# Optimization experiments

Measured on AMD Instinct MI355X. Metric: run time of the kernel, lower is better.

The kernel has to match this reference:

```python
import jax, jax.numpy as jnp
import numpy as np

B, T, D, H = 4, 1024, 1024, 16
HD = D // H
MAX_LEN = 1024


def _layernorm(x, g, b, eps=1e-5):
    mu = jnp.mean(x, axis=-1, keepdims=True)
    var = jnp.var(x, axis=-1, keepdims=True)
    return (x - mu) * jax.lax.rsqrt(var + eps) * g + b


def setup_inputs() -> dict:
    key = jax.random.key(0)
    ks = jax.random.split(key, 12)
    s = 1.0 / np.sqrt(D)
    return {
        "src": jax.random.normal(ks[0], (B, T, D), jnp.float32),
        "Wqkv": jax.random.uniform(ks[1], (D, 3 * D), jnp.float32, -s, s),
        "bqkv": jnp.zeros((3 * D,), jnp.float32),
        "Wo": jax.random.uniform(ks[2], (D, D), jnp.float32, -s, s),
        "bo": jnp.zeros((D,), jnp.float32),
        "rel_bias": 0.02 * jax.random.normal(ks[3], (H, 2 * MAX_LEN - 1), jnp.float32),
        "temperature": jnp.float32(1.0),
        "W1": jax.random.uniform(ks[4], (D, 4 * D), jnp.float32, -s, s),
        "b1": jnp.zeros((4 * D,), jnp.float32),
        "W2": jax.random.uniform(ks[5], (4 * D, D), jnp.float32, -1.0 / np.sqrt(4 * D), 1.0 / np.sqrt(4 * D)),
        "b2": jnp.zeros((D,), jnp.float32),
        "ff_scale": jnp.ones((1,), jnp.float32),
        "gamma1": jnp.ones((D,), jnp.float32),
        "beta1": jnp.zeros((D,), jnp.float32),
        "gamma2": jnp.ones((D,), jnp.float32),
        "beta2": jnp.zeros((D,), jnp.float32),
    }


def reference(src, Wqkv, bqkv, Wo, bo, rel_bias, temperature, W1, b1, W2, b2,
              ff_scale, gamma1, beta1, gamma2, beta2):
    b, t, c = src.shape
    # QKV projection -> [3, B, H, T, HD]
    qkv = (src @ Wqkv + bqkv).reshape(b, t, 3, H, HD).transpose(2, 0, 3, 1, 4)
    q, k, v = qkv[0], qkv[1], qkv[2]
    temp = jnp.maximum(temperature, 0.01)  # clamp(min=0.01)
    logits = jnp.einsum("bhqd,bhkd->bhqk", q, k) / temp
    # relative position bias gather: [H, T, T]
    pos = jnp.arange(t)
    rel = pos[None, :] - pos[:, None] + (t - 1)
    logits = logits + rel_bias[:, rel][None]
    attn_weights = jax.nn.softmax(logits, axis=-1)
    attn_out = jnp.einsum("bhqk,bhkd->bhqd", attn_weights, v)
    attn_out = attn_out.transpose(0, 2, 1, 3).reshape(b, t, c) @ Wo + bo
    x = _layernorm(src + attn_out, gamma1, beta1)
    ff = jax.nn.gelu(x @ W1 + b1, approximate=False) @ W2 + b2
    out = _layernorm(x + ff_scale * ff, gamma2, beta2)
    return (out, attn_weights)
```

## Files before the change

kernel.cpp:

```cpp
#include <hip/hip_runtime.h>
#include <math.h>

#define BB 4
#define TT 1024
#define DM 1024
#define NH 16
#define HD 64
#define DFF 4096
#define N3 3072

typedef unsigned short u16;
typedef __attribute__((ext_vector_type(4))) float f32x4;
typedef __attribute__((ext_vector_type(8))) short s16x8;

__device__ __forceinline__ u16 f2bf(float f) {
    union { float f; unsigned u; } v; v.f = f;
    unsigned u = v.u;
    u += 0x7fffu + ((u >> 16) & 1u);
    return (u16)(u >> 16);
}
__device__ __forceinline__ float bf2f(u16 h) {
    union { unsigned u; float f; } v; v.u = ((unsigned)h) << 16;
    return v.f;
}

__device__ __forceinline__ void async_copy16(const void* g, void* l) {
    __builtin_amdgcn_global_load_lds(
        (const __attribute__((address_space(1))) unsigned int*)g,
        (__attribute__((address_space(3))) unsigned int*)l, 16, 0, 0);
}

__global__ __launch_bounds__(256) void prep_kernel(const float* __restrict__ src,
                                                   u16* __restrict__ srcbf,
                                                   const float* __restrict__ Wqkv,
                                                   u16* __restrict__ WqkvT,
                                                   const float* __restrict__ Wo,
                                                   u16* __restrict__ WoT,
                                                   const float* __restrict__ W1,
                                                   u16* __restrict__ W1T,
                                                   const float* __restrict__ W2,
                                                   u16* __restrict__ W2T) {
    __shared__ float tile[32][33];
    int bid = blockIdx.x;
    int tid = threadIdx.x;
    if (bid < 4096) {
        int i = (bid * 256 + tid) * 4;
        float4 v = *(const float4*)(src + i);
        u16 pk[4] = {f2bf(v.x), f2bf(v.y), f2bf(v.z), f2bf(v.w)};
        *(uint2*)(srcbf + i) = *(uint2*)pk;
        return;
    }
    bid -= 4096;
    const float* in;
    u16* out;
    int R, C, bx, by;
    if (bid < 3072)        { in = Wqkv; out = WqkvT; R = DM;  C = N3;  bx = bid % 96;  by = bid / 96; }
    else if (bid < 4096)   { bid -= 3072; in = Wo; out = WoT; R = DM;  C = DM;  bx = bid % 32;  by = bid / 32; }
    else if (bid < 8192)   { bid -= 4096; in = W1; out = W1T; R = DM;  C = DFF; bx = bid % 128; by = bid / 128; }
    else                   { bid -= 8192; in = W2; out = W2T; R = DFF; C = DM;  bx = bid % 32;  by = bid / 32; }
    int c0 = bx * 32, r0 = by * 32;
    int tx = tid & 31, ty = tid >> 5;
    for (int i = 0; i < 4; i++)
        tile[ty + i * 8][tx] = in[(size_t)(r0 + ty + i * 8) * C + c0 + tx];
    __syncthreads();
    for (int i = 0; i < 4; i++)
        out[(size_t)(c0 + ty + i * 8) * R + r0 + tx] = f2bf(tile[tx][ty + i * 8]);
}

__global__ __launch_bounds__(256) void transpose_bf_kernel(const u16* __restrict__ inH,
                                                           u16* __restrict__ out, int R, int C) {
    __shared__ float tile[32][33];
    size_t boff = (size_t)blockIdx.z * R * C;
    int c0 = blockIdx.x * 32, r0 = blockIdx.y * 32;
    int tx = threadIdx.x & 31, ty = threadIdx.x >> 5;
    for (int i = 0; i < 4; i++) {
        int r = r0 + ty + i * 8, c = c0 + tx;
        tile[ty + i * 8][tx] = bf2f(inH[boff + (size_t)r * C + c]);
    }
    __syncthreads();
    for (int i = 0; i < 4; i++) {
        int rr = r0 + tx, cc = c0 + ty + i * 8;
        out[boff + (size_t)cc * R + rr] = f2bf(tile[tx][ty + i * 8]);
    }
}

template<int EPI, int NT>
__global__ __launch_bounds__(512, 2) void gemm256_kernel(const u16* __restrict__ A,
                                                         const u16* __restrict__ BT,
                                                         const float* __restrict__ bias,
                                                         void* __restrict__ out0v,
                                                         u16* __restrict__ out1,
                                                         u16* __restrict__ out2,
                                                         int M, int N, int Kstride) {
    __shared__ u16 As[4][8192];
    __shared__ u16 Bs[4][8192];
    const int tid = threadIdx.x;
    const int lane = tid & 63;
    const int wave = tid >> 6;
    const int quad = lane >> 4;
    const int l15 = lane & 15;
    const int wm = wave >> 2;
    const int wn = wave & 3;
    const int m0 = blockIdx.y * 256;
    const int n0 = blockIdx.x * 256;
    const int koff = blockIdx.z * (NT * 32);

    const int srow = wave * 32 + (lane >> 2);
    const int schunk = ((lane & 3) ^ ((lane >> 2) & 3)) * 8;
    const u16* aG0 = A + (size_t)(m0 + srow) * Kstride + koff + schunk;
    const u16* aG1 = aG0 + (size_t)16 * Kstride;
    const u16* bG0 = BT + (size_t)(n0 + srow) * Kstride + koff + schunk;
    const u16* bG1 = bG0 + (size_t)16 * Kstride;
    const int ldst0 = wave * 1024;
    const int ldst1 = wave * 1024 + 512;

#define STAGE_A(t) { int kk_ = (t) * 32; \
    async_copy16(aG0 + kk_, &As[(t) & 3][ldst0]); \
    async_copy16(aG1 + kk_, &As[(t) & 3][ldst1]); }
#define STAGE_B(t) { int kk_ = (t) * 32; \
    async_copy16(bG0 + kk_, &Bs[(t) & 3][ldst0]); \
    async_copy16(bG1 + kk_, &Bs[(t) & 3][ldst1]); }

    const int swq = (quad ^ (l15 & 3)) * 8;
    const int abase = (wm * 128 + l15) * 32 + swq;
    const int bbase = (wn * 64 + l15) * 32 + swq;

    f32x4 acc[8][4] = {};

    STAGE_A(0); STAGE_B(0);
    STAGE_A(1); STAGE_B(1);
    STAGE_A(2); STAGE_B(2);

#pragma unroll 1
    for (int t = 0; t < NT; ++t) {
        if (t < NT - 2)       asm volatile("s_waitcnt vmcnt(8)" ::: "memory");
        else if (t == NT - 2) asm volatile("s_waitcnt vmcnt(4)" ::: "memory");
        else                  asm volatile("s_waitcnt vmcnt(0)" ::: "memory");
        asm volatile("" ::: "memory");
        __builtin_amdgcn_s_barrier();
        asm volatile("" ::: "memory");

        const u16* as = As[t & 3];
        const u16* bs = Bs[t & 3];

        s16x8 bfr[4];
#pragma unroll
        for (int j = 0; j < 4; j++)
            bfr[j] = *(const s16x8*)&bs[bbase + j * 512];
        s16x8 afr[4];
#pragma unroll
        for (int i = 0; i < 4; i++)
            afr[i] = *(const s16x8*)&as[abase + i * 512];
        if (t + 3 < NT) STAGE_A(t + 3);
        __builtin_amdgcn_s_setprio(1);
#pragma unroll
        for (int i = 0; i < 4; i++)
#pragma unroll
            for (int j = 0; j < 4; j++)
                acc[i][j] = __builtin_amdgcn_mfma_f32_16x16x32_bf16(afr[i], bfr[j], acc[i][j], 0, 0, 0);
        __builtin_amdgcn_s_setprio(0);
#pragma unroll
        for (int i = 0; i < 4; i++)
            afr[i] = *(const s16x8*)&as[abase + 2048 + i * 512];
        if (t + 3 < NT) STAGE_B(t + 3);
        __builtin_amdgcn_s_setprio(1);
#pragma unroll
        for (int i = 0; i < 4; i++)
#pragma unroll
            for (int j = 0; j < 4; j++)
                acc[i + 4][j] = __builtin_amdgcn_mfma_f32_16x16x32_bf16(afr[i], bfr[j], acc[i + 4][j], 0, 0, 0);
        __builtin_amdgcn_s_setprio(0);
    }
#undef STAGE_A
#undef STAGE_B

    const size_t MN = (size_t)M * N;
#pragma unroll
    for (int i = 0; i < 8; i++) {
#pragma unroll
        for (int j = 0; j < 4; j++) {
            f32x4 c = acc[i][j];
            int gn = n0 + wn * 64 + j * 16 + l15;
            float bv = (EPI == 3) ? 0.f : bias[gn];
#pragma unroll
            for (int r = 0; r < 4; r++) {
                int gm = m0 + wm * 128 + i * 16 + quad * 4 + r;
                float v = c[r] + bv;
                if (EPI == 2) {
                    v = 0.5f * v * (1.f + erff(v * 0.70710678118f));
                    ((u16*)out0v)[(size_t)gm * N + gn] = f2bf(v);
                } else if (EPI == 3) {
                    ((float*)out0v)[(size_t)blockIdx.z * MN + (size_t)gm * N + gn] = v;
                } else {
                    int which = gn >> 10, h = (gn >> 6) & 15, d = gn & 63;
                    int bb = gm >> 10, tq = gm & 1023;
                    u16* dst = (which == 0) ? (u16*)out0v : ((which == 1) ? out1 : out2);
                    dst[((size_t)(bb * NH + h) * TT + tq) * HD + d] = f2bf(v);
                }
            }
        }
    }
}

__global__ __launch_bounds__(256) void attn_kernel(const u16* __restrict__ Qb,
                                                   const u16* __restrict__ Kb,
                                                   const u16* __restrict__ VTb,
                                                   const float* __restrict__ rel_bias,
                                                   const float* __restrict__ temp_p,
                                                   float* __restrict__ probs_out,
                                                   u16* __restrict__ attn_out) {
    __shared__ float RBs[1088];
    __shared__ unsigned Pl[4][16 * 20];

    const int tid = threadIdx.x;
    const int lane = tid & 63, wid = tid >> 6, quad = lane >> 4, l15 = lane & 15;
    const int q0b = blockIdx.x * 64;
    const int h = blockIdx.y, b = blockIdx.z;
    const int bh = b * NH + h;
    const size_t headoff = (size_t)bh * TT * HD;

    const float itemp = 1.f / fmaxf(temp_p[0], 0.01f);

    for (int i = tid; i < 1087; i += 256)
        RBs[i] = rel_bias[h * 2047 + (960 - q0b) + i];
    __syncthreads();

    const int qloc = wid * 16 + l15;
    const int qg = q0b + qloc;
    const u16* qp = Qb + headoff + (size_t)qg * HD;
    const s16x8 qa0 = *(const s16x8*)(qp + quad * 8);
    const s16x8 qa1 = *(const s16x8*)(qp + 32 + quad * 8);

    const u16* Kh = Kb + headoff;
    const int rbo = 63 - qloc;

    float m = -3.0e38f, l = 0.f;
#pragma unroll 2
    for (int kt = 0; kt < 64; kt++) {
        const u16* kp = Kh + (size_t)(kt * 16 + l15) * HD;
        s16x8 ka0 = *(const s16x8*)(kp + quad * 8);
        s16x8 ka1 = *(const s16x8*)(kp + 32 + quad * 8);
        f32x4 sv = {};
        sv = __builtin_amdgcn_mfma_f32_16x16x32_bf16(ka0, qa0, sv, 0, 0, 0);
        sv = __builtin_amdgcn_mfma_f32_16x16x32_bf16(ka1, qa1, sv, 0, 0, 0);
        int kb = kt * 16 + quad * 4 + rbo;
        float v0 = sv[0] * itemp + RBs[kb + 0];
        float v1 = sv[1] * itemp + RBs[kb + 1];
        float v2 = sv[2] * itemp + RBs[kb + 2];
        float v3 = sv[3] * itemp + RBs[kb + 3];
        float tm = fmaxf(fmaxf(v0, v1), fmaxf(v2, v3));
        float mn = fmaxf(m, tm);
        float c = __expf(m - mn);
        l = l * c + __expf(v0 - mn) + __expf(v1 - mn) + __expf(v2 - mn) + __expf(v3 - mn);
        m = mn;
    }
    float M = fmaxf(m, __shfl_xor(m, 16));
    M = fmaxf(M, __shfl_xor(M, 32));
    float la = l * __expf(m - M);
    la += __shfl_xor(la, 16);
    la += __shfl_xor(la, 32);
    const float inv = 1.f / la;

    f32x4 o[4] = {};
    unsigned* Pw = Pl[wid];
    const u16* Vh = VTb + headoff;
    float* prow = probs_out + ((size_t)bh * TT + qg) * TT;

#pragma unroll 1
    for (int c2 = 0; c2 < 32; c2++) {
        int k0 = c2 * 32;
#pragma unroll
        for (int t = 0; t < 2; t++) {
            int kt = 2 * c2 + t;
            const u16* kp = Kh + (size_t)(kt * 16 + l15) * HD;
            s16x8 ka0 = *(const s16x8*)(kp + quad * 8);
            s16x8 ka1 = *(const s16x8*)(kp + 32 + quad * 8);
            f32x4 sv = {};
            sv = __builtin_amdgcn_mfma_f32_16x16x32_bf16(ka0, qa0, sv, 0, 0, 0);
            sv = __builtin_amdgcn_mfma_f32_16x16x32_bf16(ka1, qa1, sv, 0, 0, 0);
            int kb = kt * 16 + quad * 4 + rbo;
            float p0 = __expf(sv[0] * itemp + RBs[kb + 0] - M) * inv;
            float p1 = __expf(sv[1] * itemp + RBs[kb + 1] - M) * inv;
            float p2 = __expf(sv[2] * itemp + RBs[kb + 2] - M) * inv;
            float p3 = __expf(sv[3] * itemp + RBs[kb + 3] - M) * inv;
            unsigned w0 = (unsigned)f2bf(p0) | ((unsigned)f2bf(p1) << 16);
            unsigned w1 = (unsigned)f2bf(p2) | ((unsigned)f2bf(p3) << 16);
            Pw[l15 * 20 + t * 8 + quad * 2 + 0] = w0;
            Pw[l15 * 20 + t * 8 + quad * 2 + 1] = w1;
        }
        s16x8 pb = *(const s16x8*)&Pw[l15 * 20 + quad * 4];
        f32x4 f0, f1;
#pragma unroll
        for (int j = 0; j < 4; j++) {
            f0[j] = bf2f((u16)pb[j]);
            f1[j] = bf2f((u16)pb[4 + j]);
        }
        *(f32x4*)(prow + k0 + quad * 8) = f0;
        *(f32x4*)(prow + k0 + quad * 8 + 4) = f1;
#pragma unroll
        for (int nt = 0; nt < 4; nt++) {
            s16x8 va = *(const s16x8*)(Vh + (size_t)(nt * 16 + l15) * TT + k0 + quad * 8);
            o[nt] = __builtin_amdgcn_mfma_f32_16x16x32_bf16(va, pb, o[nt], 0, 0, 0);
        }
    }

    u16* aout = attn_out + ((size_t)(b * TT + qg)) * DM + h * HD;
#pragma unroll
    for (int nt = 0; nt < 4; nt++) {
        u16 pk[4] = {f2bf(o[nt][0]), f2bf(o[nt][1]), f2bf(o[nt][2]), f2bf(o[nt][3])};
        *(uint2*)(aout + nt * 16 + quad * 4) = *(uint2*)pk;
    }
}

template<int MODE, int KS>
__global__ __launch_bounds__(256) void ln_kernel(const float* __restrict__ af32,
                                                 const u16* __restrict__ abf,
                                                 const float* __restrict__ part,
                                                 const float* __restrict__ biasN,
                                                 const float* __restrict__ scale_p,
                                                 const float* __restrict__ gamma,
                                                 const float* __restrict__ beta,
                                                 float* __restrict__ outf,
                                                 u16* __restrict__ outbf) {
    __shared__ float red[2][4];
    const size_t MN = (size_t)BB * TT * DM;
    int row = blockIdx.x;
    int tid = threadIdx.x;
    float sc = (MODE == 1) ? scale_p[0] : 1.f;
    int c0 = tid * 4;
    size_t base = (size_t)row * DM + c0;
    float4 a = *(const float4*)(biasN + c0);
    float acc[4] = {a.x, a.y, a.z, a.w};
#pragma unroll
    for (int kz = 0; kz < KS; kz++) {
        float4 p = *(const float4*)(part + kz * MN + base);
        acc[0] += p.x; acc[1] += p.y; acc[2] += p.z; acc[3] += p.w;
    }
    float x[4];
#pragma unroll
    for (int c = 0; c < 4; c++) {
        float b0 = (MODE == 0) ? af32[base + c] : bf2f(abf[base + c]);
        x[c] = b0 + sc * acc[c];
    }
    float s = x[0] + x[1] + x[2] + x[3];
    float sq = x[0] * x[0] + x[1] * x[1] + x[2] * x[2] + x[3] * x[3];
    for (int off = 32; off >= 1; off >>= 1) {
        s += __shfl_xor(s, off);
        sq += __shfl_xor(sq, off);
    }
    int wave = tid >> 6;
    if ((tid & 63) == 0) {
        red[0][wave] = s;
        red[1][wave] = sq;
    }
    __syncthreads();
    s = red[0][0] + red[0][1] + red[0][2] + red[0][3];
    sq = red[1][0] + red[1][1] + red[1][2] + red[1][3];
    float mu = s * (1.f / DM);
    float var = sq * (1.f / DM) - mu * mu;
    float rs = rsqrtf(var + 1e-5f);
#pragma unroll
    for (int c = 0; c < 4; c++) {
        float y = (x[c] - mu) * rs * gamma[c0 + c] + beta[c0 + c];
        if (MODE == 0) outbf[base + c] = f2bf(y);
        else outf[base + c] = y;
    }
}

#define OFF_SRCBF 0UL
#define OFF_WQKVT 8388608UL
#define OFF_WOT 14680064UL
#define OFF_W1T 16777216UL
#define OFF_W2T 25165824UL
#define OFF_Q 33554432UL
#define OFF_K 41943040UL
#define OFF_V 50331648UL
#define OFF_VT 58720256UL
#define OFF_ATTNO 67108864UL
#define OFF_XBF 83886080UL
#define OFF_H1 92274688UL
#define OFF_PART 134217728UL

extern "C" void kernel_launch(void* const* d_in, const int* in_sizes, int n_in,
                              void* d_out, int out_size, void* d_ws, size_t ws_size,
                              hipStream_t stream) {
    const float* src = (const float*)d_in[0];
    const float* Wqkv = (const float*)d_in[1];
    const float* bqkv = (const float*)d_in[2];
    const float* Wo = (const float*)d_in[3];
    const float* bo = (const float*)d_in[4];
    const float* relb = (const float*)d_in[5];
    const float* temp = (const float*)d_in[6];
    const float* W1 = (const float*)d_in[7];
    const float* b1 = (const float*)d_in[8];
    const float* W2 = (const float*)d_in[9];
    const float* b2 = (const float*)d_in[10];
    const float* ffs = (const float*)d_in[11];
    const float* g1 = (const float*)d_in[12];
    const float* be1 = (const float*)d_in[13];
    const float* g2 = (const float*)d_in[14];
    const float* be2 = (const float*)d_in[15];

    char* ws = (char*)d_ws;
    u16* srcbf = (u16*)(ws + OFF_SRCBF);
    u16* WqkvT = (u16*)(ws + OFF_WQKVT);
    u16* WoT = (u16*)(ws + OFF_WOT);
    u16* W1T = (u16*)(ws + OFF_W1T);
    u16* W2T = (u16*)(ws + OFF_W2T);
    u16* Qb = (u16*)(ws + OFF_Q);
    u16* Kb = (u16*)(ws + OFF_K);
    u16* Vb = (u16*)(ws + OFF_V);
    u16* VTb = (u16*)(ws + OFF_VT);
    u16* attnbf = (u16*)(ws + OFF_ATTNO);
    u16* xbf = (u16*)(ws + OFF_XBF);
    u16* h1bf = (u16*)(ws + OFF_H1);
    float* partF = (float*)(ws + OFF_PART);

    float* out_f = (float*)d_out;
    float* probs = out_f + (size_t)BB * TT * DM;

    prep_kernel<<<16384, 256, 0, stream>>>(src, srcbf, Wqkv, WqkvT, Wo, WoT,
                                           W1, W1T, W2, W2T);
    gemm256_kernel<1, 32><<<dim3(N3 / 256, (BB * TT) / 256, 1), 512, 0, stream>>>(
        srcbf, WqkvT, bqkv, Qb, Kb, Vb, BB * TT, N3, DM);
    transpose_bf_kernel<<<dim3(HD / 32, TT / 32, BB * NH), 256, 0, stream>>>(Vb, VTb, TT, HD);
    attn_kernel<<<dim3(TT / 64, NH, BB), 256, 0, stream>>>(Qb, Kb, VTb, relb, temp, probs, attnbf);
    gemm256_kernel<3, 8><<<dim3(DM / 256, (BB * TT) / 256, 4), 512, 0, stream>>>(
        attnbf, WoT, nullptr, partF, nullptr, nullptr, BB * TT, DM, DM);
    ln_kernel<0, 4><<<BB * TT, 256, 0, stream>>>(src, nullptr, partF, bo, nullptr, g1, be1,
                                                 nullptr, xbf);
    gemm256_kernel<2, 32><<<dim3(DFF / 256, (BB * TT) / 256, 1), 512, 0, stream>>>(
        xbf, W1T, b1, h1bf, nullptr, nullptr, BB * TT, DFF, DM);
    gemm256_kernel<3, 32><<<dim3(DM / 256, (BB * TT) / 256, 4), 512, 0, stream>>>(
        h1bf, W2T, nullptr, partF, nullptr, nullptr, BB * TT, DM, DFF);
    ln_kernel<1, 4><<<BB * TT, 256, 0, stream>>>(nullptr, xbf, partF, b2, ffs, g2, be2,
                                                 out_f, nullptr);
}
```

Measured before the change: 698.9 us.

## Stage attention probs in LDS for row-coalesced stores, remap blocks per XCD, split softmax stats

The attention kernel now buffers 256-column chunks of bf16 probabilities per wave in a larger swizzled LDS buffer, then writes each probability row out as full coalesced 1KB segments instead of scattered 32-byte pieces. The block index is remapped so consecutive blocks on the same XCD share a head's K/V data for better L2 reuse. The first-pass softmax statistics use four independent running max/sum chains with batched K loads to raise ILP. The cost is more LDS per block, which can lower occupancy, plus an extra LDS read pass for the stores.

```diff
diff --git a/kernel.cpp b/kernel.cpp
--- a/kernel.cpp
+++ b/kernel.cpp
@@ -210,12 +210,14 @@
                                                    float* __restrict__ probs_out,
                                                    u16* __restrict__ attn_out) {
     __shared__ float RBs[1088];
-    __shared__ unsigned Pl[4][16 * 20];
+    __shared__ unsigned Pc[4][16 * 132];
 
     const int tid = threadIdx.x;
     const int lane = tid & 63, wid = tid >> 6, quad = lane >> 4, l15 = lane & 15;
-    const int q0b = blockIdx.x * 64;
-    const int h = blockIdx.y, b = blockIdx.z;
+    const int bid = blockIdx.x;
+    const int lin = (bid & 7) * 128 + (bid >> 3);
+    const int q0b = (lin & 15) * 64;
+    const int h = (lin >> 4) & 15, b = lin >> 8;
     const int bh = b * NH + h;
     const size_t headoff = (size_t)bh * TT * HD;
 
@@ -234,26 +236,37 @@
     const u16* Kh = Kb + headoff;
     const int rbo = 63 - qloc;
 
-    float m = -3.0e38f, l = 0.f;
-#pragma unroll 2
-    for (int kt = 0; kt < 64; kt++) {
-        const u16* kp = Kh + (size_t)(kt * 16 + l15) * HD;
-        s16x8 ka0 = *(const s16x8*)(kp + quad * 8);
-        s16x8 ka1 = *(const s16x8*)(kp + 32 + quad * 8);
-        f32x4 sv = {};
-        sv = __builtin_amdgcn_mfma_f32_16x16x32_bf16(ka0, qa0, sv, 0, 0, 0);
-        sv = __builtin_amdgcn_mfma_f32_16x16x32_bf16(ka1, qa1, sv, 0, 0, 0);
-        int kb = kt * 16 + quad * 4 + rbo;
-        float v0 = sv[0] * itemp + RBs[kb + 0];
-        float v1 = sv[1] * itemp + RBs[kb + 1];
-        float v2 = sv[2] * itemp + RBs[kb + 2];
-        float v3 = sv[3] * itemp + RBs[kb + 3];
-        float tm = fmaxf(fmaxf(v0, v1), fmaxf(v2, v3));
-        float mn = fmaxf(m, tm);
-        float c = __expf(m - mn);
-        l = l * c + __expf(v0 - mn) + __expf(v1 - mn) + __expf(v2 - mn) + __expf(v3 - mn);
-        m = mn;
-    }
+    float pm[4] = {-3.0e38f, -3.0e38f, -3.0e38f, -3.0e38f};
+    float pl[4] = {0.f, 0.f, 0.f, 0.f};
+#pragma unroll 1
+    for (int g = 0; g < 16; g++) {
+        const u16* kp = Kh + (size_t)(g * 64 + l15) * HD;
+        s16x8 ka[8];
+#pragma unroll
+        for (int i = 0; i < 4; i++) {
+            ka[2 * i + 0] = *(const s16x8*)(kp + (size_t)i * 16 * HD + quad * 8);
+            ka[2 * i + 1] = *(const s16x8*)(kp + (size_t)i * 16 * HD + 32 + quad * 8);
+        }
+#pragma unroll
+        for (int i = 0; i < 4; i++) {
+            f32x4 sv = {};
+            sv = __builtin_amdgcn_mfma_f32_16x16x32_bf16(ka[2 * i], qa0, sv, 0, 0, 0);
+            sv = __builtin_amdgcn_mfma_f32_16x16x32_bf16(ka[2 * i + 1], qa1, sv, 0, 0, 0);
+            int kb = (g * 4 + i) * 16 + quad * 4 + rbo;
+            float v0 = sv[0] * itemp + RBs[kb + 0];
+            float v1 = sv[1] * itemp + RBs[kb + 1];
+            float v2 = sv[2] * itemp + RBs[kb + 2];
+            float v3 = sv[3] * itemp + RBs[kb + 3];
+            float tm = fmaxf(fmaxf(v0, v1), fmaxf(v2, v3));
+            float mn = fmaxf(pm[i], tm);
+            pl[i] = pl[i] * __expf(pm[i] - mn) + __expf(v0 - mn) + __expf(v1 - mn)
+                  + __expf(v2 - mn) + __expf(v3 - mn);
+            pm[i] = mn;
+        }
+    }
+    float m = fmaxf(fmaxf(pm[0], pm[1]), fmaxf(pm[2], pm[3]));
+    float l = pl[0] * __expf(pm[0] - m) + pl[1] * __expf(pm[1] - m)
+            + pl[2] * __expf(pm[2] - m) + pl[3] * __expf(pm[3] - m);
     float M = fmaxf(m, __shfl_xor(m, 16));
     M = fmaxf(M, __shfl_xor(M, 32));
     float la = l * __expf(m - M);
@@ -262,45 +275,55 @@
     const float inv = 1.f / la;
 
     f32x4 o[4] = {};
-    unsigned* Pw = Pl[wid];
+    unsigned* Pw = Pc[wid];
     const u16* Vh = VTb + headoff;
-    float* prow = probs_out + ((size_t)bh * TT + qg) * TT;
+    const int swz = (l15 & 3) << 2;
 
 #pragma unroll 1
-    for (int c2 = 0; c2 < 32; c2++) {
-        int k0 = c2 * 32;
-#pragma unroll
-        for (int t = 0; t < 2; t++) {
-            int kt = 2 * c2 + t;
-            const u16* kp = Kh + (size_t)(kt * 16 + l15) * HD;
-            s16x8 ka0 = *(const s16x8*)(kp + quad * 8);
-            s16x8 ka1 = *(const s16x8*)(kp + 32 + quad * 8);
-            f32x4 sv = {};
-            sv = __builtin_amdgcn_mfma_f32_16x16x32_bf16(ka0, qa0, sv, 0, 0, 0);
-            sv = __builtin_amdgcn_mfma_f32_16x16x32_bf16(ka1, qa1, sv, 0, 0, 0);
-            int kb = kt * 16 + quad * 4 + rbo;
-            float p0 = __expf(sv[0] * itemp + RBs[kb + 0] - M) * inv;
-            float p1 = __expf(sv[1] * itemp + RBs[kb + 1] - M) * inv;
-            float p2 = __expf(sv[2] * itemp + RBs[kb + 2] - M) * inv;
-            float p3 = __expf(sv[3] * itemp + RBs[kb + 3] - M) * inv;
-            unsigned w0 = (unsigned)f2bf(p0) | ((unsigned)f2bf(p1) << 16);
-            unsigned w1 = (unsigned)f2bf(p2) | ((unsigned)f2bf(p3) << 16);
-            Pw[l15 * 20 + t * 8 + quad * 2 + 0] = w0;
-            Pw[l15 * 20 + t * 8 + quad * 2 + 1] = w1;
+    for (int chunk = 0; chunk < 4; chunk++) {
+#pragma unroll 1
+        for (int c2l = 0; c2l < 8; c2l++) {
+            int k0g = chunk * 256 + c2l * 32;
+#pragma unroll
+            for (int t = 0; t < 2; t++) {
+                int kt = (k0g >> 4) + t;
+                const u16* kp = Kh + (size_t)(kt * 16 + l15) * HD;
+                s16x8 ka0 = *(const s16x8*)(kp + quad * 8);
+                s16x8 ka1 = *(const s16x8*)(kp + 32 + quad * 8);
+                f32x4 sv = {};
+                sv = __builtin_amdgcn_mfma_f32_16x16x32_bf16(ka0, qa0, sv, 0, 0, 0);
+                sv = __builtin_amdgcn_mfma_f32_16x16x32_bf16(ka1, qa1, sv, 0, 0, 0);
+                int kb = kt * 16 + quad * 4 + rbo;
+                float p0 = __expf(sv[0] * itemp + RBs[kb + 0] - M) * inv;
+                float p1 = __expf(sv[1] * itemp + RBs[kb + 1] - M) * inv;
+                float p2 = __expf(sv[2] * itemp + RBs[kb + 2] - M) * inv;
+                float p3 = __expf(sv[3] * itemp + RBs[kb + 3] - M) * inv;
+                unsigned w0 = (unsigned)f2bf(p0) | ((unsigned)f2bf(p1) << 16);
+                unsigned w1 = (unsigned)f2bf(p2) | ((unsigned)f2bf(p3) << 16);
+                int iw = c2l * 16 + t * 8 + quad * 2;
+                Pw[l15 * 132 + ((iw + 0) ^ swz)] = w0;
+                Pw[l15 * 132 + ((iw + 1) ^ swz)] = w1;
+            }
+            s16x8 pb = *(const s16x8*)&Pw[l15 * 132 + ((c2l * 16 + quad * 4) ^ swz)];
+#pragma unroll
+            for (int nt = 0; nt < 4; nt++) {
+                s16x8 va = *(const s16x8*)(Vh + (size_t)(nt * 16 + l15) * TT + k0g + quad * 8);
+                o[nt] = __builtin_amdgcn_mfma_f32_16x16x32_bf16(va, pb, o[nt], 0, 0, 0);
+            }
         }
-        s16x8 pb = *(const s16x8*)&Pw[l15 * 20 + quad * 4];
-        f32x4 f0, f1;
-#pragma unroll
-        for (int j = 0; j < 4; j++) {
-            f0[j] = bf2f((u16)pb[j]);
-            f1[j] = bf2f((u16)pb[4 + j]);
-        }
-        *(f32x4*)(prow + k0 + quad * 8) = f0;
-        *(f32x4*)(prow + k0 + quad * 8 + 4) = f1;
-#pragma unroll
-        for (int nt = 0; nt < 4; nt++) {
-            s16x8 va = *(const s16x8*)(Vh + (size_t)(nt * 16 + l15) * TT + k0 + quad * 8);
-            o[nt] = __builtin_amdgcn_mfma_f32_16x16x32_bf16(va, pb, o[nt], 0, 0, 0);
+#pragma unroll 1
+        for (int r16 = 0; r16 < 16; r16++) {
+            int rs = (r16 & 3) << 2;
+            unsigned v0 = Pw[r16 * 132 + ((lane * 2 + 0) ^ rs)];
+            unsigned v1 = Pw[r16 * 132 + ((lane * 2 + 1) ^ rs)];
+            f32x4 f;
+            f[0] = bf2f((u16)(v0 & 0xffff));
+            f[1] = bf2f((u16)(v0 >> 16));
+            f[2] = bf2f((u16)(v1 & 0xffff));
+            f[3] = bf2f((u16)(v1 >> 16));
+            float* pr = probs_out + ((size_t)bh * TT + q0b + wid * 16 + r16) * TT
+                      + chunk * 256 + lane * 4;
+            *(f32x4*)pr = f;
         }
     }
 
@@ -424,7 +447,7 @@
     gemm256_kernel<1, 32><<<dim3(N3 / 256, (BB * TT) / 256, 1), 512, 0, stream>>>(
         srcbf, WqkvT, bqkv, Qb, Kb, Vb, BB * TT, N3, DM);
     transpose_bf_kernel<<<dim3(HD / 32, TT / 32, BB * NH), 256, 0, stream>>>(Vb, VTb, TT, HD);
-    attn_kernel<<<dim3(TT / 64, NH, BB), 256, 0, stream>>>(Qb, Kb, VTb, relb, temp, probs, attnbf);
+    attn_kernel<<<1024, 256, 0, stream>>>(Qb, Kb, VTb, relb, temp, probs, attnbf);
     gemm256_kernel<3, 8><<<dim3(DM / 256, (BB * TT) / 256, 4), 512, 0, stream>>>(
         attnbf, WoT, nullptr, partF, nullptr, nullptr, BB * TT, DM, DM);
     ln_kernel<0, 4><<<BB * TT, 256, 0, stream>>>(src, nullptr, partF, bo, nullptr, g1, be1,
```

Result: no change. 695.1 us (-0.5%).
